# Optimization experiments

Measured on AMD Instinct MI355X. Metric: run time of the kernel, lower is better.

## Reference

```python
import jax, jax.numpy as jnp
import numpy as np

ALPHA_SCALE = 9.9
EPS_LN = 1e-5
EPS_NORM = 1e-12


def _ln(x, g, b):
    m = x.mean(axis=-1, keepdims=True)
    v = ((x - m) ** 2).mean(axis=-1, keepdims=True)
    return (x - m) / jnp.sqrt(v + EPS_LN) * g + b


def setup_inputs() -> dict:
    key = jax.random.key(0)
    ks = jax.random.split(key, 8)
    B, D, U = 32, 4096, 64
    return {
        "stimulus": jax.random.normal(ks[0], (B, D), jnp.float32),
        "prev_act": jax.random.normal(ks[1], (B, D), jnp.float32),
        "W_heb": jax.random.normal(ks[2], (D, D), jnp.float32),
        "W_rec": jax.random.normal(ks[3], (D, D), jnp.float32),
        "decay": jax.random.uniform(ks[4], (D,), jnp.float32),
        "ln_rec_g": jnp.ones((D,), jnp.float32),
        "ln_rec_b": jnp.zeros((D,), jnp.float32),
        "fc1_w": jax.random.normal(ks[5], (D, 512), jnp.float32) * 0.02,
        "fc1_b": jnp.zeros((512,), jnp.float32),
        "ln1_g": jnp.ones((512,), jnp.float32),
        "ln1_b": jnp.zeros((512,), jnp.float32),
        "fc2_w": jax.random.normal(ks[6], (512, 256), jnp.float32) * 0.05,
        "fc2_b": jnp.zeros((256,), jnp.float32),
        "ln2_g": jnp.ones((256,), jnp.float32),
        "ln2_b": jnp.zeros((256,), jnp.float32),
        "fc3_w": jax.random.normal(ks[7], (256, U), jnp.float32) * 0.05,
        "fc3_b": jnp.zeros((U,), jnp.float32),
        "lno_g": jnp.ones((U,), jnp.float32),
        "lno_b": jnp.zeros((U,), jnp.float32),
    }


def reference(stimulus, prev_act, W_heb, W_rec, decay, ln_rec_g, ln_rec_b,
              fc1_w, fc1_b, ln1_g, ln1_b, fc2_w, fc2_b, ln2_g, ln2_b,
              fc3_w, fc3_b, lno_g, lno_b):
    D = W_heb.shape[0]
    U = fc3_b.shape[0]
    # recurrent path
    rec_out = jax.nn.relu(prev_act @ W_rec)           # [B, D]
    rec_norm = _ln(rec_out, ln_rec_g, ln_rec_b)
    # stimulus path
    stim_out = jax.nn.relu(stimulus @ W_heb)          # [B, D]
    final = stim_out + rec_norm                       # [B, D]
    # neuromodulator MLP -> dopamine (mean over batch)
    h = jax.nn.relu(_ln(final @ fc1_w + fc1_b, ln1_g, ln1_b))
    h = jax.nn.relu(_ln(h @ fc2_w + fc2_b, ln2_g, ln2_b))
    dop = jnp.tanh(_ln(h @ fc3_w + fc3_b, lno_g, lno_b)).mean(axis=0)  # [U]
    alpha = jnp.repeat(dop, D // U) * ALPHA_SCALE                      # [D]
    # Hebbian updates: batched outer products accumulated = GEMM
    heb_upd = jnp.einsum('bi,bj->ij', stimulus, stim_out)   # [D, D]
    rec_upd = jnp.einsum('bi,bj->ij', prev_act, rec_out)    # [D, D]
    W1 = W_heb + heb_upd * alpha[None, :]
    W2 = W_rec + rec_upd * alpha[None, :]
    # decay: W - diag(decay) @ W == (1 - decay) row-scale
    W1 = W1 * (1.0 - decay)[:, None]
    W2 = W2 * (1.0 - decay)[:, None]
    # row-wise L2 normalize (F.normalize p=2 dim=1)
    W1 = W1 / jnp.maximum(jnp.linalg.norm(W1, axis=1, keepdims=True), EPS_NORM)
    W2 = W2 / jnp.maximum(jnp.linalg.norm(W2, axis=1, keepdims=True), EPS_NORM)
    # [B+2D, D]: final_output followed by the two updated weight buffers
    return jnp.concatenate([final, W1, W2], axis=0)
```

## Files before the change

kernel.cpp:

```cpp
#include <hip/hip_runtime.h>
#include <stdint.h>

typedef unsigned short ushort_t;
typedef float f32x4 __attribute__((ext_vector_type(4)));
typedef short s16x8 __attribute__((ext_vector_type(8)));

#define B_  32
#define D_  4096
#define H1_ 512
#define H2_ 256
#define U_  64

#define KS_   16
#define KCH_  256
#define NT_   256
#define APAD  264
#define WPAD  72

__device__ __forceinline__ float bf2f(ushort_t u) {
    return __uint_as_float(((uint32_t)u) << 16);
}
__device__ __forceinline__ ushort_t f2bfu(float f) {
    uint32_t x = __float_as_uint(f);
    return (ushort_t)((x + 0x7fffu + ((x >> 16) & 1u)) >> 16);
}
__device__ __forceinline__ uint32_t pk2bf(float a, float b) {
    return ((uint32_t)f2bfu(a)) | (((uint32_t)f2bfu(b)) << 16);
}

__global__ __launch_bounds__(256, 2) void k_gemm_mfma(
    const float* __restrict__ stim, const float* __restrict__ prev,
    const float* __restrict__ Wheb, const float* __restrict__ Wrec,
    float* __restrict__ Psum)
{
    __shared__ ushort_t Al[32 * APAD];
    __shared__ ushort_t Wt[NT_ * WPAD];

    int bx = blockIdx.x;
    int gemm  = bx >> 8;
    int rem   = bx & 255;
    int nblk  = rem >> 4;
    int chunk = rem & 15;
    const float* A = gemm ? prev : stim;
    const float* W = gemm ? Wrec : Wheb;
    int k0c = chunk * KCH_;
    int n0  = nblk * NT_;
    int tid = threadIdx.x, lane = tid & 63, wave = tid >> 6;
    int col = lane & 15, quad = lane >> 4;

#pragma unroll
    for (int p = 0; p < 16; p++) {
        int idx = p * 256 + tid;
        int b   = idx >> 7;
        int kk  = (idx & 127) * 2;
        float2 v = *(const float2*)(A + (size_t)b * D_ + k0c + kk);
        *(uint32_t*)&Al[b * APAD + kk] = pk2bf(v.x, v.y);
    }

    f32x4 acc[2][4];
#pragma unroll
    for (int mt = 0; mt < 2; mt++)
#pragma unroll
        for (int nt = 0; nt < 4; nt++)
            acc[mt][nt] = (f32x4){0.f, 0.f, 0.f, 0.f};

    for (int ks = 0; ks < 4; ks++) {
        __syncthreads();
        const float* Wc = W + (size_t)(k0c + ks * 64) * D_ + n0 + tid;
        uint32_t* dst = (uint32_t*)&Wt[tid * WPAD];
#pragma unroll
        for (int i = 0; i < 32; i++) {
            float a = Wc[(size_t)(2 * i) * D_];
            float b = Wc[(size_t)(2 * i + 1) * D_];
            dst[i] = pk2bf(a, b);
        }
        __syncthreads();

#pragma unroll
        for (int kq = 0; kq < 2; kq++) {
            int kb = ks * 64 + kq * 32 + quad * 8;
            int kw = kq * 32 + quad * 8;
            s16x8 af[2], bf[4];
            af[0] = *(const s16x8*)&Al[col * APAD + kb];
            af[1] = *(const s16x8*)&Al[(col + 16) * APAD + kb];
#pragma unroll
            for (int nt = 0; nt < 4; nt++)
                bf[nt] = *(const s16x8*)&Wt[(wave * 64 + nt * 16 + col) * WPAD + kw];
#pragma unroll
            for (int mt = 0; mt < 2; mt++)
#pragma unroll
                for (int nt = 0; nt < 4; nt++)
                    acc[mt][nt] = __builtin_amdgcn_mfma_f32_16x16x32_bf16(
                        af[mt], bf[nt], acc[mt][nt], 0, 0, 0);
        }
    }

    float* P = Psum + (size_t)gemm * 32 * D_;
#pragma unroll
    for (int mt = 0; mt < 2; mt++)
#pragma unroll
        for (int nt = 0; nt < 4; nt++)
#pragma unroll
            for (int r = 0; r < 4; r++) {
                int b = mt * 16 + quad * 4 + r;
                int n = n0 + wave * 64 + nt * 16 + col;
                atomicAdd(&P[(size_t)b * D_ + n], acc[mt][nt][r]);
            }
}

__global__ __launch_bounds__(256) void k_reduce(
    const float* __restrict__ Psum,
    const float* __restrict__ stim, const float* __restrict__ prev,
    float* __restrict__ P_relu, ushort_t* __restrict__ Tbuf)
{
    int idx = blockIdx.x * 256 + threadIdx.x;
    int gemm = idx >> 17;
    int r    = idx & 131071;
    int b    = r >> 12;
    int d    = r & 4095;
    float s = fmaxf(Psum[idx], 0.f);
    P_relu[idx] = s;
    Tbuf[(2 + gemm) * 131072 + d * 32 + b] = f2bfu(s);
    Tbuf[gemm * 131072 + d * 32 + b] = f2bfu((gemm ? prev : stim)[r]);
}

__global__ __launch_bounds__(256) void k_final_ln(
    const float* __restrict__ P_relu,
    const float* __restrict__ g, const float* __restrict__ be,
    float* __restrict__ dout, float* __restrict__ finalf32)
{
    __shared__ float red[256], red2[256];
    int b = blockIdx.x, tid = threadIdx.x;
    const float* rec = P_relu + 131072 + b * D_;
    const float* stm = P_relu + b * D_;

    float s = 0.f, s2 = 0.f;
    for (int d = tid; d < D_; d += 256) { float x = rec[d]; s += x; s2 += x * x; }
    red[tid] = s; red2[tid] = s2; __syncthreads();
    for (int st = 128; st > 0; st >>= 1) {
        if (tid < st) { red[tid] += red[tid + st]; red2[tid] += red2[tid + st]; }
        __syncthreads();
    }
    float m = red[0] * (1.f / D_);
    float v = red2[0] * (1.f / D_) - m * m;
    float rstd = rsqrtf(v + 1e-5f);

    for (int d = tid; d < D_; d += 256) {
        float fn = stm[d] + (rec[d] - m) * rstd * g[d] + be[d];
        finalf32[b * D_ + d] = fn;
        dout[b * D_ + d] = fn;
    }
}

__global__ __launch_bounds__(256) void k_fc1(
    const float* __restrict__ finalf32, const float* __restrict__ fc1w,
    float* __restrict__ z1p)
{
    int kc = blockIdx.x;
    int t  = threadIdx.x;
    int k0 = kc * 64;
    const float2* W2 = (const float2*)fc1w;

    float a0[32], a1[32];
#pragma unroll
    for (int b = 0; b < 32; b++) { a0[b] = 0.f; a1[b] = 0.f; }

    for (int k = k0; k < k0 + 64; k++) {
        float2 wv = W2[k * (H1_ / 2) + t];
#pragma unroll
        for (int b = 0; b < 32; b++) {
            float a = finalf32[b * D_ + k];
            a0[b] = fmaf(a, wv.x, a0[b]);
            a1[b] = fmaf(a, wv.y, a1[b]);
        }
    }
    float* P = z1p + (size_t)kc * 32 * H1_;
#pragma unroll
    for (int b = 0; b < 32; b++) {
        P[b * H1_ + 2 * t]     = a0[b];
        P[b * H1_ + 2 * t + 1] = a1[b];
    }
}

__global__ __launch_bounds__(256) void k_tail(
    const float* __restrict__ z1p,
    const float* __restrict__ fc1b,
    const float* __restrict__ ln1g, const float* __restrict__ ln1b,
    const float* __restrict__ fc2w, const float* __restrict__ fc2b,
    const float* __restrict__ ln2g, const float* __restrict__ ln2b,
    const float* __restrict__ fc3w, const float* __restrict__ fc3b,
    const float* __restrict__ lnog, const float* __restrict__ lnob,
    float* __restrict__ tanhout)
{
    __shared__ float sm[512];
    __shared__ float red[256], red2[256];
    __shared__ float h2s[256];
    int b = blockIdx.x, tid = threadIdx.x;

    for (int j = tid; j < H1_; j += 256) {
        float s = fc1b[j];
        for (int c = 0; c < 64; c++)
            s += z1p[((size_t)c * 32 + b) * H1_ + j];
        sm[j] = s;
    }
    __syncthreads();

    float s = 0.f, s2 = 0.f;
    for (int j = tid; j < H1_; j += 256) { float x = sm[j]; s += x; s2 += x * x; }
    red[tid] = s; red2[tid] = s2; __syncthreads();
    for (int st = 128; st > 0; st >>= 1) {
        if (tid < st) { red[tid] += red[tid + st]; red2[tid] += red2[tid + st]; }
        __syncthreads();
    }
    float m = red[0] * (1.f / H1_);
    float v = red2[0] * (1.f / H1_) - m * m;
    float rstd = rsqrtf(v + 1e-5f);
    __syncthreads();
    for (int j = tid; j < H1_; j += 256) {
        float h = (sm[j] - m) * rstd * ln1g[j] + ln1b[j];
        sm[j] = fmaxf(h, 0.f);
    }
    __syncthreads();

    float acc = fc2b[tid];
    for (int k = 0; k < H1_; k++)
        acc = fmaf(sm[k], fc2w[k * H2_ + tid], acc);
    red[tid] = acc; red2[tid] = acc * acc; __syncthreads();
    for (int st = 128; st > 0; st >>= 1) {
        if (tid < st) { red[tid] += red[tid + st]; red2[tid] += red2[tid + st]; }
        __syncthreads();
    }
    float m2 = red[0] * (1.f / H2_);
    float v2 = red2[0] * (1.f / H2_) - m2 * m2;
    float rstd2 = rsqrtf(v2 + 1e-5f);
    float h2 = fmaxf((acc - m2) * rstd2 * ln2g[tid] + ln2b[tid], 0.f);
    __syncthreads();
    h2s[tid] = h2; __syncthreads();

    int j  = tid & 63;
    int ks = tid >> 6;
    float p = 0.f;
    for (int kk = 0; kk < 64; kk++) {
        int k = ks * 64 + kk;
        p = fmaf(h2s[k], fc3w[k * U_ + j], p);
    }
    red[tid] = p; __syncthreads();
    if (tid < 64) {
        float x = red[tid] + red[tid + 64] + red[tid + 128] + red[tid + 192]
                + fc3b[tid];
        float ss = x, qq = x * x;
#pragma unroll
        for (int off = 32; off; off >>= 1) {
            ss += __shfl_xor(ss, off, 64);
            qq += __shfl_xor(qq, off, 64);
        }
        float m3 = ss * (1.f / U_);
        float v3 = qq * (1.f / U_) - m3 * m3;
        float to = tanhf((x - m3) * rsqrtf(v3 + 1e-5f) * lnog[tid] + lnob[tid]);
        tanhout[b * U_ + tid] = to;
    }
}

__global__ __launch_bounds__(256) void k_update(
    const float* __restrict__ Wheb, const float* __restrict__ Wrec,
    const float* __restrict__ decay, const float* __restrict__ tanhout,
    const ushort_t* __restrict__ Tbuf, float* __restrict__ dout)
{
    __shared__ ushort_t cache[8 * 4096];
    int bx = blockIdx.x;
    int mat   = bx >> 9;
    int itile = bx & 511;
    int i0    = itile * 8;
    int tid  = threadIdx.x;
    int wv   = tid >> 6;
    int lane = tid & 63;
    int ir0 = i0 + wv * 2, ir1 = ir0 + 1;

    float al = 0.f;
#pragma unroll
    for (int b = 0; b < 32; b++) al += tanhout[b * U_ + lane];
    al *= (9.9f / 32.f);

    const ushort_t* Sp = Tbuf + mat * 131072;
    const uint4* s0p = (const uint4*)(Sp + (size_t)ir0 * 32);
    const uint4* s1p = (const uint4*)(Sp + (size_t)ir1 * 32);
    float st0[32], st1[32];
#pragma unroll
    for (int q = 0; q < 4; q++) {
        uint4 a = s0p[q], c = s1p[q];
        const uint32_t aw[4] = {a.x, a.y, a.z, a.w};
        const uint32_t cw[4] = {c.x, c.y, c.z, c.w};
#pragma unroll
        for (int e = 0; e < 4; e++) {
            st0[q * 8 + 2 * e]     = __uint_as_float(aw[e] << 16);
            st0[q * 8 + 2 * e + 1] = __uint_as_float(aw[e] & 0xffff0000u);
            st1[q * 8 + 2 * e]     = __uint_as_float(cw[e] << 16);
            st1[q * 8 + 2 * e + 1] = __uint_as_float(cw[e] & 0xffff0000u);
        }
    }
    float dc0 = 1.f - decay[ir0];
    float dc1 = 1.f - decay[ir1];

    const ushort_t* Op = Tbuf + (2 + mat) * 131072;
    const float* Wp = mat ? Wrec : Wheb;

    float ss0 = 0.f, ss1 = 0.f;
    for (int jt = 0; jt < 64; jt++) {
        int j = jt * 64 + lane;
        float av = __shfl(al, jt, 64);
        const uint4* op = (const uint4*)(Op + (size_t)j * 32);
        float u0 = 0.f, u1 = 0.f;
#pragma unroll
        for (int q = 0; q < 4; q++) {
            uint4 a = op[q];
            const uint32_t w4[4] = {a.x, a.y, a.z, a.w};
#pragma unroll
            for (int e = 0; e < 4; e++) {
                float o0 = __uint_as_float(w4[e] << 16);
                float o1 = __uint_as_float(w4[e] & 0xffff0000u);
                u0 = fmaf(st0[q * 8 + 2 * e], o0, u0);
                u0 = fmaf(st0[q * 8 + 2 * e + 1], o1, u0);
                u1 = fmaf(st1[q * 8 + 2 * e], o0, u1);
                u1 = fmaf(st1[q * 8 + 2 * e + 1], o1, u1);
            }
        }
        float w0v = Wp[(size_t)ir0 * D_ + j];
        float w1v = Wp[(size_t)ir1 * D_ + j];
        float v0 = (w0v + av * u0) * dc0;
        float v1 = (w1v + av * u1) * dc1;
        ss0 += v0 * v0;
        ss1 += v1 * v1;
        cache[(wv * 2) * 4096 + j]     = f2bfu(v0);
        cache[(wv * 2 + 1) * 4096 + j] = f2bfu(v1);
    }
#pragma unroll
    for (int off = 32; off; off >>= 1) {
        ss0 += __shfl_xor(ss0, off, 64);
        ss1 += __shfl_xor(ss1, off, 64);
    }
    float ri0 = 1.f / fmaxf(sqrtf(ss0), 1e-12f);
    float ri1 = 1.f / fmaxf(sqrtf(ss1), 1e-12f);

    float* O0 = dout + (size_t)(32 + mat * D_ + ir0) * D_;
    float* O1 = O0 + D_;
    for (int j = lane; j < D_; j += 64) {
        O0[j] = bf2f(cache[(wv * 2) * 4096 + j]) * ri0;
        O1[j] = bf2f(cache[(wv * 2 + 1) * 4096 + j]) * ri1;
    }
}

extern "C" void kernel_launch(void* const* d_in, const int* in_sizes, int n_in,
                              void* d_out, int out_size, void* d_ws, size_t ws_size,
                              hipStream_t stream)
{
    const float* stim = (const float*)d_in[0];
    const float* prev = (const float*)d_in[1];
    const float* Wheb = (const float*)d_in[2];
    const float* Wrec = (const float*)d_in[3];
    const float* decay= (const float*)d_in[4];
    const float* lnrg = (const float*)d_in[5];
    const float* lnrb = (const float*)d_in[6];
    const float* fc1w = (const float*)d_in[7];
    const float* fc1b = (const float*)d_in[8];
    const float* ln1g = (const float*)d_in[9];
    const float* ln1b = (const float*)d_in[10];
    const float* fc2w = (const float*)d_in[11];
    const float* fc2b = (const float*)d_in[12];
    const float* ln2g = (const float*)d_in[13];
    const float* ln2b = (const float*)d_in[14];
    const float* fc3w = (const float*)d_in[15];
    const float* fc3b = (const float*)d_in[16];
    const float* lnog = (const float*)d_in[17];
    const float* lnob = (const float*)d_in[18];

    char* ws = (char*)d_ws;
    float*    P_sum   = (float*)(ws + 0);
    float*    P_relu  = (float*)(ws + 1048576);
    ushort_t* P_tbuf  = (ushort_t*)(ws + 2097152);
    float*    P_final = (float*)(ws + 3145728);
    float*    P_z1p   = (float*)(ws + 3670016);
    float*    P_tanh  = (float*)(ws + 7864320);

    float* out = (float*)d_out;

    hipMemsetAsync(P_sum, 0, 2 * 32 * D_ * sizeof(float), stream);

    k_gemm_mfma<<<512,  256, 0, stream>>>(stim, prev, Wheb, Wrec, P_sum);
    k_reduce   <<<1024, 256, 0, stream>>>(P_sum, stim, prev, P_relu, P_tbuf);
    k_final_ln <<<32,   256, 0, stream>>>(P_relu, lnrg, lnrb, out, P_final);
    k_fc1      <<<64,   256, 0, stream>>>(P_final, fc1w, P_z1p);
    k_tail     <<<32,   256, 0, stream>>>(P_z1p, fc1b, ln1g, ln1b, fc2w, fc2b,
                                          ln2g, ln2b, fc3w, fc3b, lnog, lnob, P_tanh);
    k_update   <<<1024, 256, 0, stream>>>(Wheb, Wrec, decay, P_tanh, P_tbuf, out);
}
```

Before: 479.0 us.

## Halve GEMM N-tile and replace split-K atomics with per-slice partial buffers

```diff
diff --git a/kernel.cpp b/kernel.cpp
--- a/kernel.cpp
+++ b/kernel.cpp
@@ -13,7 +13,7 @@
 
 #define KS_   16
 #define KCH_  256
-#define NT_   256
+#define NT_   128
 #define APAD  264
 #define WPAD  72
 
@@ -28,17 +28,17 @@
     return ((uint32_t)f2bfu(a)) | (((uint32_t)f2bfu(b)) << 16);
 }
 
-__global__ __launch_bounds__(256, 2) void k_gemm_mfma(
+__global__ __launch_bounds__(256, 4) void k_gemm_mfma(
     const float* __restrict__ stim, const float* __restrict__ prev,
     const float* __restrict__ Wheb, const float* __restrict__ Wrec,
-    float* __restrict__ Psum)
+    float* __restrict__ Psum, int ns)
 {
     __shared__ ushort_t Al[32 * APAD];
     __shared__ ushort_t Wt[NT_ * WPAD];
 
     int bx = blockIdx.x;
-    int gemm  = bx >> 8;
-    int rem   = bx & 255;
+    int gemm  = bx >> 9;
+    int rem   = bx & 511;
     int nblk  = rem >> 4;
     int chunk = rem & 15;
     const float* A = gemm ? prev : stim;
@@ -57,19 +57,22 @@
         *(uint32_t*)&Al[b * APAD + kk] = pk2bf(v.x, v.y);
     }
 
-    f32x4 acc[2][4];
+    f32x4 acc[2][2];
 #pragma unroll
     for (int mt = 0; mt < 2; mt++)
 #pragma unroll
-        for (int nt = 0; nt < 4; nt++)
+        for (int nt = 0; nt < 2; nt++)
             acc[mt][nt] = (f32x4){0.f, 0.f, 0.f, 0.f};
+
+    int wcol = tid & 127;
+    int kh   = (tid >> 7) * 32;
 
     for (int ks = 0; ks < 4; ks++) {
         __syncthreads();
-        const float* Wc = W + (size_t)(k0c + ks * 64) * D_ + n0 + tid;
-        uint32_t* dst = (uint32_t*)&Wt[tid * WPAD];
-#pragma unroll
-        for (int i = 0; i < 32; i++) {
+        const float* Wc = W + (size_t)(k0c + ks * 64 + kh) * D_ + n0 + wcol;
+        uint32_t* dst = (uint32_t*)&Wt[wcol * WPAD] + (kh >> 1);
+#pragma unroll
+        for (int i = 0; i < 16; i++) {
             float a = Wc[(size_t)(2 * i) * D_];
             float b = Wc[(size_t)(2 * i + 1) * D_];
             dst[i] = pk2bf(a, b);
@@ -80,45 +83,62 @@
         for (int kq = 0; kq < 2; kq++) {
             int kb = ks * 64 + kq * 32 + quad * 8;
             int kw = kq * 32 + quad * 8;
-            s16x8 af[2], bf[4];
+            s16x8 af[2], bf[2];
             af[0] = *(const s16x8*)&Al[col * APAD + kb];
             af[1] = *(const s16x8*)&Al[(col + 16) * APAD + kb];
 #pragma unroll
-            for (int nt = 0; nt < 4; nt++)
-                bf[nt] = *(const s16x8*)&Wt[(wave * 64 + nt * 16 + col) * WPAD + kw];
+            for (int nt = 0; nt < 2; nt++)
+                bf[nt] = *(const s16x8*)&Wt[(wave * 32 + nt * 16 + col) * WPAD + kw];
 #pragma unroll
             for (int mt = 0; mt < 2; mt++)
 #pragma unroll
-                for (int nt = 0; nt < 4; nt++)
+                for (int nt = 0; nt < 2; nt++)
                     acc[mt][nt] = __builtin_amdgcn_mfma_f32_16x16x32_bf16(
                         af[mt], bf[nt], acc[mt][nt], 0, 0, 0);
         }
     }
 
-    float* P = Psum + (size_t)gemm * 32 * D_;
-#pragma unroll
-    for (int mt = 0; mt < 2; mt++)
-#pragma unroll
-        for (int nt = 0; nt < 4; nt++)
-#pragma unroll
-            for (int r = 0; r < 4; r++) {
-                int b = mt * 16 + quad * 4 + r;
-                int n = n0 + wave * 64 + nt * 16 + col;
-                atomicAdd(&P[(size_t)b * D_ + n], acc[mt][nt][r]);
-            }
+    int slice = chunk % ns;
+    float* P = Psum + ((size_t)slice * 2 + gemm) * 32 * D_;
+    if (ns == 16) {
+#pragma unroll
+        for (int mt = 0; mt < 2; mt++)
+#pragma unroll
+            for (int nt = 0; nt < 2; nt++)
+#pragma unroll
+                for (int r = 0; r < 4; r++) {
+                    int b = mt * 16 + quad * 4 + r;
+                    int n = n0 + wave * 32 + nt * 16 + col;
+                    P[(size_t)b * D_ + n] = acc[mt][nt][r];
+                }
+    } else {
+#pragma unroll
+        for (int mt = 0; mt < 2; mt++)
+#pragma unroll
+            for (int nt = 0; nt < 2; nt++)
+#pragma unroll
+                for (int r = 0; r < 4; r++) {
+                    int b = mt * 16 + quad * 4 + r;
+                    int n = n0 + wave * 32 + nt * 16 + col;
+                    atomicAdd(&P[(size_t)b * D_ + n], acc[mt][nt][r]);
+                }
+    }
 }
 
 __global__ __launch_bounds__(256) void k_reduce(
     const float* __restrict__ Psum,
     const float* __restrict__ stim, const float* __restrict__ prev,
-    float* __restrict__ P_relu, ushort_t* __restrict__ Tbuf)
+    float* __restrict__ P_relu, ushort_t* __restrict__ Tbuf, int ns)
 {
     int idx = blockIdx.x * 256 + threadIdx.x;
     int gemm = idx >> 17;
     int r    = idx & 131071;
     int b    = r >> 12;
     int d    = r & 4095;
-    float s = fmaxf(Psum[idx], 0.f);
+    float s = 0.f;
+    for (int sl = 0; sl < ns; sl++)
+        s += Psum[((size_t)sl * 2 + gemm) * 131072 + r];
+    s = fmaxf(s, 0.f);
     P_relu[idx] = s;
     Tbuf[(2 + gemm) * 131072 + d * 32 + b] = f2bfu(s);
     Tbuf[gemm * 131072 + d * 32 + b] = f2bfu((gemm ? prev : stim)[r]);
@@ -373,20 +393,31 @@
     const float* lnog = (const float*)d_in[17];
     const float* lnob = (const float*)d_in[18];
 
+    const size_t FIXED = 1048576u + 1048576u + 524288u + 4194304u + 8192u;
+    int ns = 16;
+    if (ws_size < FIXED + 16u * 1048576u) {
+        size_t avail = (ws_size > FIXED) ? (ws_size - FIXED) / 1048576u : 1u;
+        ns = (int)avail;
+        if (ns < 1) ns = 1;
+        if (ns > 16) ns = 16;
+    }
+
     char* ws = (char*)d_ws;
     float*    P_sum   = (float*)(ws + 0);
-    float*    P_relu  = (float*)(ws + 1048576);
-    ushort_t* P_tbuf  = (ushort_t*)(ws + 2097152);
-    float*    P_final = (float*)(ws + 3145728);
-    float*    P_z1p   = (float*)(ws + 3670016);
-    float*    P_tanh  = (float*)(ws + 7864320);
+    char*     rest    = ws + (size_t)ns * 1048576u;
+    float*    P_relu  = (float*)(rest + 0);
+    ushort_t* P_tbuf  = (ushort_t*)(rest + 1048576);
+    float*    P_final = (float*)(rest + 2097152);
+    float*    P_z1p   = (float*)(rest + 2621440);
+    float*    P_tanh  = (float*)(rest + 6815744);
 
     float* out = (float*)d_out;
 
-    hipMemsetAsync(P_sum, 0, 2 * 32 * D_ * sizeof(float), stream);
-
-    k_gemm_mfma<<<512,  256, 0, stream>>>(stim, prev, Wheb, Wrec, P_sum);
-    k_reduce   <<<1024, 256, 0, stream>>>(P_sum, stim, prev, P_relu, P_tbuf);
+    if (ns < 16)
+        hipMemsetAsync(P_sum, 0, (size_t)ns * 1048576u, stream);
+
+    k_gemm_mfma<<<1024, 256, 0, stream>>>(stim, prev, Wheb, Wrec, P_sum, ns);
+    k_reduce   <<<1024, 256, 0, stream>>>(P_sum, stim, prev, P_relu, P_tbuf, ns);
     k_final_ln <<<32,   256, 0, stream>>>(P_relu, lnrg, lnrb, out, P_final);
     k_fc1      <<<64,   256, 0, stream>>>(P_final, fc1w, P_z1p);
     k_tail     <<<32,   256, 0, stream>>>(P_z1p, fc1b, ln1g, ln1b, fc2w, fc2b,
```

Result: faster. 424.9 us (-11.3%).
